# Performance work log

Hardware: AMD Instinct MI355X
Metric: run time of the kernel (lower is better)

## Reference

```python
import jax, jax.numpy as jnp
import numpy as np


def setup_inputs() -> dict:
    key = jax.random.key(0)
    k1, k2, k3 = jax.random.split(key, 3)
    N, K, C, M = 16, 32768, 16, 128
    pred_boxes = jax.random.normal(k1, (N, K, 5), dtype=jnp.float32)
    pred_cls = jax.random.normal(k2, (N, K, C), dtype=jnp.float32)
    target = jax.random.uniform(k3, (N, M, 5), dtype=jnp.float32)
    return {"pred_boxes": pred_boxes, "pred_cls": pred_cls, "target": target}


def _losses(pred_boxes, pred_cls, target):
    N, K, _ = pred_boxes.shape
    M = target.shape[1]
    C = pred_cls.shape[2]
    mask = target.sum(axis=2) != 0                      # (N, M)
    maskf = mask.astype(pred_boxes.dtype)
    denom = maskf.sum()
    tboxes = target[..., 1:]                            # (N, M, 4) corners (x1,y1,x2,y2)
    tcls = target[..., 0].astype(jnp.int32)             # (N, M)
    pconf = pred_boxes[..., 4]                          # (N, K)
    pb = pred_boxes[..., :4]                            # (N, K, 4) (x, y, w, h)

    # pred corners (N, 1, K)
    p_x1 = pb[:, None, :, 0]
    p_y1 = pb[:, None, :, 1]
    p_x2 = (pb[..., 2] + pb[..., 0])[:, None, :]
    p_y2 = (pb[..., 3] + pb[..., 1])[:, None, :]
    # target corners (N, M, 1)
    t_x1 = tboxes[..., 0:1]
    t_y1 = tboxes[..., 1:2]
    t_x2 = tboxes[..., 2:3]
    t_y2 = tboxes[..., 3:4]

    ix1 = jnp.maximum(p_x1, t_x1)
    iy1 = jnp.maximum(p_y1, t_y1)
    ix2 = jnp.minimum(p_x2, t_x2)
    iy2 = jnp.minimum(p_y2, t_y2)
    inter = jnp.clip(ix2 - ix1 + 1, 0) * jnp.clip(iy2 - iy1 + 1, 0)   # (N, M, K)
    a1 = (p_x2 - p_x1 + 1) * (p_y2 - p_y1 + 1)
    a2 = (t_x2 - t_x1 + 1) * (t_y2 - t_y1 + 1)
    iou = inter / (a1 + a2 - inter + 1e-16)

    best = jnp.argmax(iou, axis=-1)                     # (N, M)
    best_idx = jnp.where(mask, best, 0)                 # masked targets keep index 0 (as torch init)

    best_pb = jnp.take_along_axis(pb, best_idx[..., None], axis=1)       # (N, M, 4)
    best_cls = jnp.take_along_axis(pred_cls, best_idx[..., None], axis=1)  # (N, M, C)
    # NOTE: faithful to original: conf gather indices are never updated -> always index 0
    conf_idx = jnp.zeros((N, M), dtype=jnp.int32)
    best_conf = jax.nn.sigmoid(jnp.take_along_axis(pconf, conf_idx, axis=1))  # (N, M)

    def masked_mean(v):
        return (v * maskf).sum() / denom

    logp = jax.nn.log_softmax(best_cls, axis=-1)
    ce = -jnp.take_along_axis(logp, tcls[..., None], axis=-1)[..., 0]
    loss_cls = masked_mean(ce)

    loss_x = masked_mean((best_pb[..., 0] - tboxes[..., 0]) ** 2)
    loss_y = masked_mean((best_pb[..., 1] - tboxes[..., 1]) ** 2)
    loss_w = masked_mean((best_pb[..., 2] - (tboxes[..., 2] - tboxes[..., 0])) ** 2)
    loss_h = masked_mean((best_pb[..., 3] - (tboxes[..., 3] - tboxes[..., 1])) ** 2)

    labels = (best_conf > 0.5).astype(best_conf.dtype)
    bce = -(labels * jnp.log(best_conf) + (1.0 - labels) * jnp.log(1.0 - best_conf))
    loss_conf = masked_mean(bce)

    loss = loss_cls + loss_x + loss_y + loss_w + loss_h + loss_conf
    return loss, loss_cls, loss_x, loss_y, loss_w, loss_h, loss_conf


def reference(pred_boxes, pred_cls, target):
    return _losses(pred_boxes, pred_cls, target)
```

## Files before the change

kernel.cpp:

```cpp
#include <hip/hip_runtime.h>
#include <hip/hip_bf16.h>
#include <math.h>

constexpr int N_ = 16;
constexpr int K_ = 32768;
constexpr int C_ = 16;
constexpr int M_ = 128;

constexpr int KC = 256;
constexpr int CHUNKS = K_ / KC;
constexpr int WAVES = 4;
constexpr int KSL = KC / WAVES;

#define POISON_I ((int)0xAAAAAAAAu)

__device__ __forceinline__ unsigned long long load_agent_u64(
    const unsigned long long* p) {
  return __hip_atomic_load(p, __ATOMIC_RELAXED, __HIP_MEMORY_SCOPE_AGENT);
}
__device__ __forceinline__ void store_agent_f32(float* p, float v) {
  __hip_atomic_store(p, v, __ATOMIC_RELAXED, __HIP_MEMORY_SCOPE_AGENT);
}
__device__ __forceinline__ float load_agent_f32(const float* p) {
  return __hip_atomic_load(p, __ATOMIC_RELAXED, __HIP_MEMORY_SCOPE_AGENT);
}

__global__ __launch_bounds__(256, 8) void fused_loss_kernel(
    const float* __restrict__ pred_boxes,
    const float* __restrict__ pred_cls,
    const float* __restrict__ target,
    unsigned long long* __restrict__ rowmin,
    float* __restrict__ ws2,
    int* __restrict__ cnt,
    float* __restrict__ out) {
  __shared__ float4 lds4[KC];
  __shared__ float piou_s[WAVES][M_];
  __shared__ int pidx_s[WAVES][M_];
  __shared__ float red[4][7];
  __shared__ int s_flag;

  const int chunk = blockIdx.x;
  const int n = blockIdx.y;
  const int k0 = chunk * KC;
  const int tid = threadIdx.x;

  {
    const float* p = pred_boxes + ((size_t)(n * K_ + k0 + tid)) * 5;
    const float x = p[0];
    const float y = p[1];
    const float bw = p[2];
    const float bh = p[3];
    const float px2 = bw + x;
    const float py2 = bh + y;
    lds4[tid] = make_float4(x, y, px2 + 1.0f, py2 + 1.0f);
  }
  __syncthreads();

  const int wv = tid >> 6;
  const int lane = tid & 63;
  const int m0 = lane;
  const int m1 = lane + 64;

  const float* tgA = target + ((size_t)(n * M_ + m0)) * 5;
  const float tx1A = tgA[1];
  const float ty1A = tgA[2];
  const float tx2A = tgA[3] + 1.0f;
  const float ty2A = tgA[4] + 1.0f;
  const float a2A = (tgA[3] - tgA[1] + 1.0f) * (tgA[4] - tgA[2] + 1.0f) + 1e-16f;

  const float* tgB = target + ((size_t)(n * M_ + m1)) * 5;
  const float tx1B = tgB[1];
  const float ty1B = tgB[2];
  const float tx2B = tgB[3] + 1.0f;
  const float ty2B = tgB[4] + 1.0f;
  const float a2B = (tgB[3] - tgB[1] + 1.0f) * (tgB[4] - tgB[2] + 1.0f) + 1e-16f;

  float bestA = -INFINITY, bestB = -INFINITY;
  int bkA = 0, bkB = 0;

  const int ks = wv * KSL;
  const int ke = ks + KSL;
#pragma unroll 4
  for (int kl = ks; kl < ke; ++kl) {
    const float4 v = lds4[kl];
    const float a1 = (v.z - v.x) * (v.w - v.y);
    {
      float ww = fminf(v.z, tx2A) - fmaxf(v.x, tx1A);
      float hh = fminf(v.w, ty2A) - fmaxf(v.y, ty1A);
      ww = fmaxf(ww, 0.0f);
      hh = fmaxf(hh, 0.0f);
      const float inter = ww * hh;
      const float iou = inter * __builtin_amdgcn_rcpf((a1 + a2A) - inter);
      const bool gt = iou > bestA;
      bestA = gt ? iou : bestA;
      bkA = gt ? kl : bkA;
    }
    {
      float ww = fminf(v.z, tx2B) - fmaxf(v.x, tx1B);
      float hh = fminf(v.w, ty2B) - fmaxf(v.y, ty1B);
      ww = fmaxf(ww, 0.0f);
      hh = fmaxf(hh, 0.0f);
      const float inter = ww * hh;
      const float iou = inter * __builtin_amdgcn_rcpf((a1 + a2B) - inter);
      const bool gt = iou > bestB;
      bestB = gt ? iou : bestB;
      bkB = gt ? kl : bkB;
    }
  }

  piou_s[wv][m0] = bestA;
  pidx_s[wv][m0] = bkA;
  piou_s[wv][m1] = bestB;
  pidx_s[wv][m1] = bkB;
  __syncthreads();

  if (tid < M_) {
    float b = piou_s[0][tid];
    int bi = pidx_s[0][tid];
#pragma unroll
    for (int w2 = 1; w2 < WAVES; ++w2) {
      const float v = piou_s[w2][tid];
      const int id = pidx_s[w2][tid];
      const bool gt = v > b;
      b = gt ? v : b;
      bi = gt ? id : bi;
    }
    const unsigned kb = __float_as_uint(b);
    const unsigned ord = kb ^ (unsigned)(((int)kb >> 31) | 0x80000000);
    const unsigned long long ikey =
        ((unsigned long long)(~ord) << 32) | (unsigned)(k0 + bi);
    atomicMin(&rowmin[(size_t)n * M_ + tid], ikey);
  }

  __syncthreads();
  if (tid == 0) {
    const int old = atomicAdd(&cnt[n], 1);
    s_flag = (old == POISON_I + (CHUNKS - 1)) || (old == CHUNKS - 1);
  }
  __syncthreads();
  if (!s_flag) return;

  {
    const int m = tid & (M_ - 1);
    float acc[7] = {0, 0, 0, 0, 0, 0, 0};
    if (tid < M_) {
      const unsigned long long pk =
          load_agent_u64(&rowmin[(size_t)n * M_ + m]);
      const int bidx0 = (int)(unsigned)pk;

      const float* tg2 = target + ((size_t)(n * M_ + m)) * 5;
      const float t0 = tg2[0], t1 = tg2[1], t2 = tg2[2], t3 = tg2[3],
                  t4 = tg2[4];
      const float sum5 = t0 + t1 + t2 + t3 + t4;
      const float mk = (sum5 != 0.0f) ? 1.0f : 0.0f;
      const int bidx = (sum5 != 0.0f) ? bidx0 : 0;

      const float* pb = pred_boxes + ((size_t)(n * K_ + bidx)) * 5;
      const float b0 = pb[0], b1 = pb[1], bw = pb[2], bh = pb[3];

      const float4* pc =
          (const float4*)(pred_cls + ((size_t)(n * K_ + bidx)) * C_);
      float vals[C_];
#pragma unroll
      for (int q = 0; q < 4; ++q) {
        const float4 vv = pc[q];
        vals[q * 4 + 0] = vv.x;
        vals[q * 4 + 1] = vv.y;
        vals[q * 4 + 2] = vv.z;
        vals[q * 4 + 3] = vv.w;
      }
      int tcls = (int)t0;
      tcls = tcls < 0 ? 0 : (tcls >= C_ ? C_ - 1 : tcls);
      float mx = -INFINITY;
#pragma unroll
      for (int q = 0; q < C_; ++q) mx = fmaxf(mx, vals[q]);
      float se = 0.0f;
#pragma unroll
      for (int q = 0; q < C_; ++q) se += expf(vals[q] - mx);
      const float ce2 = logf(se) + mx - vals[tcls];

      const float dx = b0 - t1;
      const float dy = b1 - t2;
      const float dw = bw - (t3 - t1);
      const float dh = bh - (t4 - t2);

      const float pcf = pred_boxes[(size_t)n * K_ * 5 + 4];
      const float bc = 1.0f / (1.0f + expf(-pcf));
      const float bce = (bc > 0.5f) ? -logf(bc) : -logf(1.0f - bc);

      acc[0] = mk;
      acc[1] = mk * ce2;
      acc[2] = mk * dx * dx;
      acc[3] = mk * dy * dy;
      acc[4] = mk * dw * dw;
      acc[5] = mk * dh * dh;
      acc[6] = mk * bce;
    }

#pragma unroll
    for (int i = 0; i < 7; ++i) {
      float v = acc[i];
      for (int off = 32; off > 0; off >>= 1) v += __shfl_down(v, off, 64);
      acc[i] = v;
    }
    const int lane2 = tid & 63;
    const int wid = tid >> 6;
    if (lane2 == 0) {
#pragma unroll
      for (int i = 0; i < 7; ++i) red[wid][i] = acc[i];
    }
    __syncthreads();

    if (tid == 0) {
#pragma unroll
      for (int i = 0; i < 7; ++i)
        store_agent_f32(&ws2[n * 8 + i],
                        red[0][i] + red[1][i] + red[2][i] + red[3][i]);
    }
    __syncthreads();
    if (tid == 0) {
      const int old2 = atomicAdd(&cnt[N_], 1);
      s_flag = (old2 == POISON_I + (N_ - 1)) || (old2 == N_ - 1);
    }
    __syncthreads();
  }

  if (s_flag && tid == 0) {
    float s[7] = {0, 0, 0, 0, 0, 0, 0};
    for (int nn = 0; nn < N_; ++nn)
#pragma unroll
      for (int i = 0; i < 7; ++i) s[i] += load_agent_f32(&ws2[nn * 8 + i]);
    const float denom = s[0];
    const float lc = s[1] / denom;
    const float lx = s[2] / denom;
    const float ly = s[3] / denom;
    const float lw = s[4] / denom;
    const float lh = s[5] / denom;
    const float lf = s[6] / denom;
    out[0] = lc + lx + ly + lw + lh + lf;
    out[1] = lc;
    out[2] = lx;
    out[3] = ly;
    out[4] = lw;
    out[5] = lh;
    out[6] = lf;
  }
}

extern "C" void kernel_launch(void* const* d_in, const int* in_sizes, int n_in,
                              void* d_out, int out_size, void* d_ws, size_t ws_size,
                              hipStream_t stream) {
  const float* pred_boxes = (const float*)d_in[0];
  const float* pred_cls = (const float*)d_in[1];
  const float* target = (const float*)d_in[2];
  float* out = (float*)d_out;

  unsigned long long* rowmin = (unsigned long long*)d_ws;
  float* ws2 = (float*)(rowmin + (size_t)N_ * M_);
  int* cnt = (int*)(ws2 + N_ * 8);

  dim3 g(CHUNKS, N_);
  fused_loss_kernel<<<g, 256, 0, stream>>>(pred_boxes, pred_cls, target,
                                           rowmin, ws2, cnt, out);
}
```

Measured before the change: 120.3 us.

## Make each wave independent: per-wave atomicMin and completion counting without block barriers

Each wave now stages its own 64 predicted boxes in a private LDS slice and publishes its per-target best IoU via global 64-bit atomicMin directly, dropping the shared-memory cross-wave reduction and all __syncthreads. Completion detection moves to a per-wave counter so the last wave per image performs the gather/loss and the final cross-image reduction. This removes block-level barriers at the cost of four times as many global atomics on the same row addresses and more counter traffic.

```diff
diff --git a/kernel.cpp b/kernel.cpp
--- a/kernel.cpp
+++ b/kernel.cpp
@@ -1,5 +1,4 @@
 #include <hip/hip_runtime.h>
-#include <hip/hip_bf16.h>
 #include <math.h>
 
 constexpr int N_ = 16;
@@ -7,12 +6,13 @@
 constexpr int C_ = 16;
 constexpr int M_ = 128;
 
-constexpr int KC = 256;
-constexpr int CHUNKS = K_ / KC;
-constexpr int WAVES = 4;
-constexpr int KSL = KC / WAVES;
-
-#define POISON_I ((int)0xAAAAAAAAu)
+constexpr int KW = 64;
+constexpr int WPB = 4;
+constexpr int KB = KW * WPB;
+constexpr int BLOCKS_PER_N = K_ / KB;
+constexpr int WAVES_PER_N = BLOCKS_PER_N * WPB;
+
+#define POISON_U 0xAAAAAAAAu
 
 __device__ __forceinline__ unsigned long long load_agent_u64(
     const unsigned long long* p) {
@@ -33,42 +33,31 @@
     float* __restrict__ ws2,
     int* __restrict__ cnt,
     float* __restrict__ out) {
-  __shared__ float4 lds4[KC];
-  __shared__ float piou_s[WAVES][M_];
-  __shared__ int pidx_s[WAVES][M_];
-  __shared__ float red[4][7];
-  __shared__ int s_flag;
-
-  const int chunk = blockIdx.x;
+  __shared__ float4 lds4[KB];
+
+  const int tid = threadIdx.x;
+  const int wv = tid >> 6;
+  const int lane = tid & 63;
   const int n = blockIdx.y;
-  const int k0 = chunk * KC;
-  const int tid = threadIdx.x;
+  const int k0 = blockIdx.x * KB + wv * KW;
 
   {
-    const float* p = pred_boxes + ((size_t)(n * K_ + k0 + tid)) * 5;
+    const float* p = pred_boxes + ((size_t)(n * K_ + k0 + lane)) * 5;
     const float x = p[0];
     const float y = p[1];
     const float bw = p[2];
     const float bh = p[3];
-    const float px2 = bw + x;
-    const float py2 = bh + y;
-    lds4[tid] = make_float4(x, y, px2 + 1.0f, py2 + 1.0f);
-  }
-  __syncthreads();
-
-  const int wv = tid >> 6;
-  const int lane = tid & 63;
-  const int m0 = lane;
-  const int m1 = lane + 64;
-
-  const float* tgA = target + ((size_t)(n * M_ + m0)) * 5;
+    lds4[wv * KW + lane] = make_float4(x, y, bw + x + 1.0f, bh + y + 1.0f);
+  }
+
+  const float* tgA = target + ((size_t)(n * M_ + lane)) * 5;
   const float tx1A = tgA[1];
   const float ty1A = tgA[2];
   const float tx2A = tgA[3] + 1.0f;
   const float ty2A = tgA[4] + 1.0f;
   const float a2A = (tgA[3] - tgA[1] + 1.0f) * (tgA[4] - tgA[2] + 1.0f) + 1e-16f;
 
-  const float* tgB = target + ((size_t)(n * M_ + m1)) * 5;
+  const float* tgB = target + ((size_t)(n * M_ + lane + 64)) * 5;
   const float tx1B = tgB[1];
   const float ty1B = tgB[2];
   const float tx2B = tgB[3] + 1.0f;
@@ -78,11 +67,9 @@
   float bestA = -INFINITY, bestB = -INFINITY;
   int bkA = 0, bkB = 0;
 
-  const int ks = wv * KSL;
-  const int ke = ks + KSL;
 #pragma unroll 4
-  for (int kl = ks; kl < ke; ++kl) {
-    const float4 v = lds4[kl];
+  for (int kl = 0; kl < KW; ++kl) {
+    const float4 v = lds4[wv * KW + kl];
     const float a1 = (v.z - v.x) * (v.w - v.y);
     {
       float ww = fminf(v.z, tx2A) - fmaxf(v.x, tx1A);
@@ -108,142 +95,112 @@
     }
   }
 
-  piou_s[wv][m0] = bestA;
-  pidx_s[wv][m0] = bkA;
-  piou_s[wv][m1] = bestB;
-  pidx_s[wv][m1] = bkB;
-  __syncthreads();
-
-  if (tid < M_) {
-    float b = piou_s[0][tid];
-    int bi = pidx_s[0][tid];
-#pragma unroll
-    for (int w2 = 1; w2 < WAVES; ++w2) {
-      const float v = piou_s[w2][tid];
-      const int id = pidx_s[w2][tid];
-      const bool gt = v > b;
-      b = gt ? v : b;
-      bi = gt ? id : bi;
-    }
-    const unsigned kb = __float_as_uint(b);
-    const unsigned ord = kb ^ (unsigned)(((int)kb >> 31) | 0x80000000);
-    const unsigned long long ikey =
-        ((unsigned long long)(~ord) << 32) | (unsigned)(k0 + bi);
-    atomicMin(&rowmin[(size_t)n * M_ + tid], ikey);
-  }
-
-  __syncthreads();
-  if (tid == 0) {
-    const int old = atomicAdd(&cnt[n], 1);
-    s_flag = (old == POISON_I + (CHUNKS - 1)) || (old == CHUNKS - 1);
-  }
-  __syncthreads();
-  if (!s_flag) return;
-
   {
-    const int m = tid & (M_ - 1);
-    float acc[7] = {0, 0, 0, 0, 0, 0, 0};
-    if (tid < M_) {
-      const unsigned long long pk =
-          load_agent_u64(&rowmin[(size_t)n * M_ + m]);
-      const int bidx0 = (int)(unsigned)pk;
-
-      const float* tg2 = target + ((size_t)(n * M_ + m)) * 5;
-      const float t0 = tg2[0], t1 = tg2[1], t2 = tg2[2], t3 = tg2[3],
-                  t4 = tg2[4];
-      const float sum5 = t0 + t1 + t2 + t3 + t4;
-      const float mk = (sum5 != 0.0f) ? 1.0f : 0.0f;
-      const int bidx = (sum5 != 0.0f) ? bidx0 : 0;
-
-      const float* pb = pred_boxes + ((size_t)(n * K_ + bidx)) * 5;
-      const float b0 = pb[0], b1 = pb[1], bw = pb[2], bh = pb[3];
-
-      const float4* pc =
-          (const float4*)(pred_cls + ((size_t)(n * K_ + bidx)) * C_);
-      float vals[C_];
-#pragma unroll
-      for (int q = 0; q < 4; ++q) {
-        const float4 vv = pc[q];
-        vals[q * 4 + 0] = vv.x;
-        vals[q * 4 + 1] = vv.y;
-        vals[q * 4 + 2] = vv.z;
-        vals[q * 4 + 3] = vv.w;
-      }
-      int tcls = (int)t0;
-      tcls = tcls < 0 ? 0 : (tcls >= C_ ? C_ - 1 : tcls);
-      float mx = -INFINITY;
-#pragma unroll
-      for (int q = 0; q < C_; ++q) mx = fmaxf(mx, vals[q]);
-      float se = 0.0f;
-#pragma unroll
-      for (int q = 0; q < C_; ++q) se += expf(vals[q] - mx);
-      const float ce2 = logf(se) + mx - vals[tcls];
-
-      const float dx = b0 - t1;
-      const float dy = b1 - t2;
-      const float dw = bw - (t3 - t1);
-      const float dh = bh - (t4 - t2);
-
-      const float pcf = pred_boxes[(size_t)n * K_ * 5 + 4];
-      const float bc = 1.0f / (1.0f + expf(-pcf));
-      const float bce = (bc > 0.5f) ? -logf(bc) : -logf(1.0f - bc);
-
-      acc[0] = mk;
-      acc[1] = mk * ce2;
-      acc[2] = mk * dx * dx;
-      acc[3] = mk * dy * dy;
-      acc[4] = mk * dw * dw;
-      acc[5] = mk * dh * dh;
-      acc[6] = mk * bce;
-    }
-
-#pragma unroll
-    for (int i = 0; i < 7; ++i) {
-      float v = acc[i];
-      for (int off = 32; off > 0; off >>= 1) v += __shfl_down(v, off, 64);
-      acc[i] = v;
-    }
-    const int lane2 = tid & 63;
-    const int wid = tid >> 6;
-    if (lane2 == 0) {
-#pragma unroll
-      for (int i = 0; i < 7; ++i) red[wid][i] = acc[i];
-    }
-    __syncthreads();
-
-    if (tid == 0) {
-#pragma unroll
-      for (int i = 0; i < 7; ++i)
-        store_agent_f32(&ws2[n * 8 + i],
-                        red[0][i] + red[1][i] + red[2][i] + red[3][i]);
-    }
-    __syncthreads();
-    if (tid == 0) {
-      const int old2 = atomicAdd(&cnt[N_], 1);
-      s_flag = (old2 == POISON_I + (N_ - 1)) || (old2 == N_ - 1);
-    }
-    __syncthreads();
-  }
-
-  if (s_flag && tid == 0) {
-    float s[7] = {0, 0, 0, 0, 0, 0, 0};
-    for (int nn = 0; nn < N_; ++nn)
-#pragma unroll
-      for (int i = 0; i < 7; ++i) s[i] += load_agent_f32(&ws2[nn * 8 + i]);
-    const float denom = s[0];
-    const float lc = s[1] / denom;
-    const float lx = s[2] / denom;
-    const float ly = s[3] / denom;
-    const float lw = s[4] / denom;
-    const float lh = s[5] / denom;
-    const float lf = s[6] / denom;
-    out[0] = lc + lx + ly + lw + lh + lf;
-    out[1] = lc;
-    out[2] = lx;
-    out[3] = ly;
-    out[4] = lw;
-    out[5] = lh;
-    out[6] = lf;
+    const unsigned kbA = __float_as_uint(bestA);
+    const unsigned ordA = kbA ^ (unsigned)(((int)kbA >> 31) | 0x80000000);
+    atomicMin(&rowmin[(size_t)n * M_ + lane],
+              ((unsigned long long)(~ordA) << 32) | (unsigned)(k0 + bkA));
+    const unsigned kbB = __float_as_uint(bestB);
+    const unsigned ordB = kbB ^ (unsigned)(((int)kbB >> 31) | 0x80000000);
+    atomicMin(&rowmin[(size_t)n * M_ + lane + 64],
+              ((unsigned long long)(~ordB) << 32) | (unsigned)(k0 + bkB));
+  }
+
+  __builtin_amdgcn_s_waitcnt(0);
+  int old = 0;
+  if (lane == 0) old = atomicAdd(&cnt[n], 1);
+  old = __shfl(old, 0, 64);
+  const unsigned uo = (unsigned)old;
+  if (!(uo == POISON_U + (WAVES_PER_N - 1) || uo == WAVES_PER_N - 1)) return;
+
+  float acc[7] = {0, 0, 0, 0, 0, 0, 0};
+#pragma unroll
+  for (int r = 0; r < 2; ++r) {
+    const int m = lane + r * 64;
+    const unsigned long long pk = load_agent_u64(&rowmin[(size_t)n * M_ + m]);
+    const int bidx0 = (int)(unsigned)pk;
+
+    const float* tg2 = target + ((size_t)(n * M_ + m)) * 5;
+    const float t0 = tg2[0], t1 = tg2[1], t2 = tg2[2], t3 = tg2[3],
+                t4 = tg2[4];
+    const float sum5 = t0 + t1 + t2 + t3 + t4;
+    const float mk = (sum5 != 0.0f) ? 1.0f : 0.0f;
+    const int bidx = (sum5 != 0.0f) ? bidx0 : 0;
+
+    const float* pb = pred_boxes + ((size_t)(n * K_ + bidx)) * 5;
+    const float b0 = pb[0], b1 = pb[1], bw = pb[2], bh = pb[3];
+
+    const float4* pc =
+        (const float4*)(pred_cls + ((size_t)(n * K_ + bidx)) * C_);
+    float vals[C_];
+#pragma unroll
+    for (int q = 0; q < 4; ++q) {
+      const float4 vv = pc[q];
+      vals[q * 4 + 0] = vv.x;
+      vals[q * 4 + 1] = vv.y;
+      vals[q * 4 + 2] = vv.z;
+      vals[q * 4 + 3] = vv.w;
+    }
+    int tcls = (int)t0;
+    tcls = tcls < 0 ? 0 : (tcls >= C_ ? C_ - 1 : tcls);
+    float mx = -INFINITY;
+#pragma unroll
+    for (int q = 0; q < C_; ++q) mx = fmaxf(mx, vals[q]);
+    float se = 0.0f;
+#pragma unroll
+    for (int q = 0; q < C_; ++q) se += expf(vals[q] - mx);
+    const float ce2 = logf(se) + mx - vals[tcls];
+
+    const float dx = b0 - t1;
+    const float dy = b1 - t2;
+    const float dw = bw - (t3 - t1);
+    const float dh = bh - (t4 - t2);
+
+    const float pcf = pred_boxes[(size_t)n * K_ * 5 + 4];
+    const float bc = 1.0f / (1.0f + expf(-pcf));
+    const float bce = (bc > 0.5f) ? -logf(bc) : -logf(1.0f - bc);
+
+    acc[0] += mk;
+    acc[1] += mk * ce2;
+    acc[2] += mk * dx * dx;
+    acc[3] += mk * dy * dy;
+    acc[4] += mk * dw * dw;
+    acc[5] += mk * dh * dh;
+    acc[6] += mk * bce;
+  }
+
+#pragma unroll
+  for (int i = 0; i < 7; ++i) {
+    float v = acc[i];
+    for (int off = 32; off > 0; off >>= 1) v += __shfl_down(v, off, 64);
+    acc[i] = v;
+  }
+
+  if (lane == 0) {
+#pragma unroll
+    for (int i = 0; i < 7; ++i) store_agent_f32(&ws2[n * 8 + i], acc[i]);
+    __builtin_amdgcn_s_waitcnt(0);
+    const unsigned old2 = (unsigned)atomicAdd(&cnt[N_], 1);
+    if (old2 == POISON_U + (N_ - 1) || old2 == N_ - 1) {
+      float s[7] = {0, 0, 0, 0, 0, 0, 0};
+      for (int nn = 0; nn < N_; ++nn)
+#pragma unroll
+        for (int i = 0; i < 7; ++i) s[i] += load_agent_f32(&ws2[nn * 8 + i]);
+      const float denom = s[0];
+      const float lc = s[1] / denom;
+      const float lx = s[2] / denom;
+      const float ly = s[3] / denom;
+      const float lw = s[4] / denom;
+      const float lh = s[5] / denom;
+      const float lf = s[6] / denom;
+      out[0] = lc + lx + ly + lw + lh + lf;
+      out[1] = lc;
+      out[2] = lx;
+      out[3] = ly;
+      out[4] = lw;
+      out[5] = lh;
+      out[6] = lf;
+    }
   }
 }
 
@@ -259,7 +216,7 @@
   float* ws2 = (float*)(rowmin + (size_t)N_ * M_);
   int* cnt = (int*)(ws2 + N_ * 8);
 
-  dim3 g(CHUNKS, N_);
+  dim3 g(BLOCKS_PER_N, N_);
   fused_loss_kernel<<<g, 256, 0, stream>>>(pred_boxes, pred_cls, target,
                                            rowmin, ws2, cnt, out);
 }
```

Measured after the change: 188.9 us. 1.57x slower.
